# Kernel optimization log

Measured on AMD Instinct MI355X. Metric: run time of the kernel, lower is better.

The kernel has to match this reference:

```python
import jax, jax.numpy as jnp
import numpy as np

N_NODES = 100000


def gcn_conv(x, edge_index, W, b, n_nodes):
    """PyG GCNConv: add self-loops, symmetric deg^-1/2 normalization,
    linear transform, scatter-add aggregate, bias."""
    src, dst = edge_index[0], edge_index[1]
    # add self-loops
    loop = jnp.arange(n_nodes, dtype=edge_index.dtype)
    src = jnp.concatenate([src, loop])
    dst = jnp.concatenate([dst, loop])
    # transform first (in_dim >= out_dim ordering used by PyG)
    h = x @ W  # [N, out]
    # symmetric normalization from in-degree (incl. self-loops)
    ones = jnp.ones(src.shape[0], dtype=x.dtype)
    deg = jax.ops.segment_sum(ones, dst, num_segments=n_nodes)
    dinv = jnp.where(deg > 0, jax.lax.rsqrt(deg), 0.0).astype(x.dtype)
    norm = dinv[src] * dinv[dst]  # [E+N]
    msg = h[src] * norm[:, None]  # gather + scale
    out = jax.ops.segment_sum(msg, dst, num_segments=n_nodes)
    return out + b


def setup_inputs() -> dict:
    key = jax.random.key(0)
    k1, k2, k3, k4 = jax.random.split(key, 4)
    n, e = N_NODES, 1600000
    d_in, d_hid, n_cls = 256, 256, 64
    x = jax.random.normal(k1, (n, d_in), dtype=jnp.float32)
    edge_index = jax.random.randint(k2, (2, e), 0, n, dtype=jnp.int64)
    W1 = jax.random.normal(k3, (d_in, d_hid), dtype=jnp.float32) / np.sqrt(d_in)
    b1 = jnp.zeros((d_hid,), dtype=jnp.float32)
    W2 = jax.random.normal(k4, (d_hid, n_cls), dtype=jnp.float32) / np.sqrt(d_hid)
    b2 = jnp.zeros((n_cls,), dtype=jnp.float32)
    return {"x": x, "edge_index": edge_index, "W1": W1, "b1": b1, "W2": W2, "b2": b2}


def reference(x, edge_index, W1, b1, W2, b2):
    n = x.shape[0]
    h = jax.nn.relu(gcn_conv(x, edge_index, W1, b1, n))
    # dropout is identity in eval mode (training=False)
    logits = gcn_conv(h, edge_index, W2, b2, n)
    return jax.nn.log_softmax(logits, axis=1)
```

## Files before the change

kernel.cpp:

```cpp
#include <hip/hip_runtime.h>
#include <math.h>


typedef __attribute__((ext_vector_type(8))) short bf16x8;
typedef __attribute__((ext_vector_type(4))) float f32x4;

__device__ inline unsigned short f2bf(float f) {
    union { float f; unsigned int u; } v; v.f = f;
    unsigned int r = v.u + 0x7fffu + ((v.u >> 16) & 1u);
    return (unsigned short)(r >> 16);
}
__device__ inline float bf2f_lo(unsigned int u) {
    union { unsigned int u; float f; } v; v.u = u << 16; return v.f;
}
__device__ inline float bf2f_hi(unsigned int u) {
    union { unsigned int u; float f; } v; v.u = u & 0xffff0000u; return v.f;
}

__device__ inline void acc8(float* acc, uint4 q, float w) {
    acc[0] += bf2f_lo(q.x) * w; acc[1] += bf2f_hi(q.x) * w;
    acc[2] += bf2f_lo(q.y) * w; acc[3] += bf2f_hi(q.y) * w;
    acc[4] += bf2f_lo(q.z) * w; acc[5] += bf2f_hi(q.z) * w;
    acc[6] += bf2f_lo(q.w) * w; acc[7] += bf2f_hi(q.w) * w;
}

__global__ __launch_bounds__(256) void deg_count_kernel(
    const int* __restrict__ dst, int E, int* __restrict__ cnt) {
    int e = blockIdx.x * blockDim.x + threadIdx.x;
    if (e < E) atomicAdd(&cnt[dst[e]], 1);
}

__global__ __launch_bounds__(256) void scan_part1_kernel(
    const int* __restrict__ cnt, int* __restrict__ bsum, int N) {
    __shared__ int s[256];
    const int tid = threadIdx.x;
    int base = blockIdx.x * 1024 + tid * 4;
    int v = 0;
#pragma unroll
    for (int j = 0; j < 4; ++j)
        if (base + j < N) v += cnt[base + j];
    s[tid] = v;
    __syncthreads();
    for (int off = 128; off > 0; off >>= 1) {
        if (tid < off) s[tid] += s[tid + off];
        __syncthreads();
    }
    if (tid == 0) bsum[blockIdx.x] = s[0];
}

__global__ __launch_bounds__(1024) void scan_part2_kernel(
    const int* __restrict__ bsum, int* __restrict__ boffs, int NB,
    int* __restrict__ row_ptr, int N) {
    __shared__ int s[1024];
    const int tid = threadIdx.x;
    int v = (tid < NB) ? bsum[tid] : 0;
    s[tid] = v;
    __syncthreads();
    for (int off = 1; off < 1024; off <<= 1) {
        int t = (tid >= off) ? s[tid - off] : 0;
        __syncthreads();
        if (tid >= off) s[tid] += t;
        __syncthreads();
    }
    if (tid < NB) boffs[tid] = s[tid] - v;
    if (tid == 1023) row_ptr[N] = s[1023];
}

__global__ __launch_bounds__(256) void scan_part3_kernel(
    const int* __restrict__ cnt, const int* __restrict__ boffs,
    int* __restrict__ row_ptr, int* __restrict__ cursor, int N) {
    __shared__ int s[256];
    const int tid = threadIdx.x;
    int base = blockIdx.x * 1024 + tid * 4;
    int c[4];
    int v = 0;
#pragma unroll
    for (int j = 0; j < 4; ++j) {
        c[j] = (base + j < N) ? cnt[base + j] : 0;
        v += c[j];
    }
    s[tid] = v;
    __syncthreads();
    for (int off = 1; off < 256; off <<= 1) {
        int t = (tid >= off) ? s[tid - off] : 0;
        __syncthreads();
        if (tid >= off) s[tid] += t;
        __syncthreads();
    }
    int run = boffs[blockIdx.x] + s[tid] - v;
#pragma unroll
    for (int j = 0; j < 4; ++j) {
        if (base + j < N) {
            row_ptr[base + j] = run;
            cursor[base + j] = run;
            run += c[j];
        }
    }
}

__global__ __launch_bounds__(256) void scatter_kernel(
    const int* __restrict__ src, const int* __restrict__ dst,
    const int* __restrict__ cnt, int* __restrict__ cursor,
    int2* __restrict__ csr_ew, int E) {
    int e = blockIdx.x * blockDim.x + threadIdx.x;
    if (e >= E) return;
    int s = src[e], d = dst[e];
    float w = rsqrtf((float)cnt[s] + 1.0f) * rsqrtf((float)cnt[d] + 1.0f);
    int pos = atomicAdd(&cursor[d], 1);
    int2 rec;
    rec.x = s;
    rec.y = __float_as_int(w);
    csr_ew[pos] = rec;
}

__global__ __launch_bounds__(256) void castw_kernel(
    const float* __restrict__ W, unsigned short* __restrict__ Wt,
    int K, int Ncol) {
    int i = blockIdx.x * 256 + threadIdx.x;
    if (i < K * Ncol) {
        int n = i / K;
        int k = i - n * K;
        Wt[i] = f2bf(W[(size_t)k * Ncol + n]);
    }
}

__global__ __launch_bounds__(256) void gemm1_kernel(
    const float* __restrict__ A, const unsigned short* __restrict__ Bt,
    unsigned short* __restrict__ C, int M) {
    __shared__ unsigned short As[64][32];
    __shared__ unsigned short Bs[256][32];

    const int tid = threadIdx.x;
    const int wave = tid >> 6, lane = tid & 63;
    const int quad = lane >> 4, l15 = lane & 15;
    const int m0 = blockIdx.x * 64;

    f32x4 acc[4][4] = {};

    const int arow = tid >> 2;
    const int akk = (tid & 3) << 3;
    const int gr = m0 + arow;

    for (int k0 = 0; k0 < 256; k0 += 32) {
        float4 a0 = make_float4(0.f, 0.f, 0.f, 0.f), a1 = a0;
        if (gr < M) {
            a0 = *(const float4*)&A[(size_t)gr * 256 + k0 + akk];
            a1 = *(const float4*)&A[(size_t)gr * 256 + k0 + akk + 4];
        }
        bf16x8 av;
        av[0] = (short)f2bf(a0.x); av[1] = (short)f2bf(a0.y);
        av[2] = (short)f2bf(a0.z); av[3] = (short)f2bf(a0.w);
        av[4] = (short)f2bf(a1.x); av[5] = (short)f2bf(a1.y);
        av[6] = (short)f2bf(a1.z); av[7] = (short)f2bf(a1.w);
        *(bf16x8*)&As[arow][akk] = av;

        const unsigned short* bsrc = &Bt[(size_t)tid * 256 + k0];
        *(bf16x8*)&Bs[tid][0]  = *(const bf16x8*)&bsrc[0];
        *(bf16x8*)&Bs[tid][8]  = *(const bf16x8*)&bsrc[8];
        *(bf16x8*)&Bs[tid][16] = *(const bf16x8*)&bsrc[16];
        *(bf16x8*)&Bs[tid][24] = *(const bf16x8*)&bsrc[24];
        __syncthreads();

        bf16x8 af[4], bfv[4];
#pragma unroll
        for (int mt = 0; mt < 4; ++mt)
            af[mt] = *(const bf16x8*)&As[mt * 16 + l15][quad * 8];
#pragma unroll
        for (int nt = 0; nt < 4; ++nt)
            bfv[nt] = *(const bf16x8*)&Bs[wave * 64 + nt * 16 + l15][quad * 8];
#pragma unroll
        for (int mt = 0; mt < 4; ++mt)
#pragma unroll
            for (int nt = 0; nt < 4; ++nt)
                acc[mt][nt] = __builtin_amdgcn_mfma_f32_16x16x32_bf16(
                    af[mt], bfv[nt], acc[mt][nt], 0, 0, 0);
        __syncthreads();
    }

#pragma unroll
    for (int mt = 0; mt < 4; ++mt) {
#pragma unroll
        for (int nt = 0; nt < 4; ++nt) {
            int gcol = wave * 64 + nt * 16 + l15;
#pragma unroll
            for (int r = 0; r < 4; ++r) {
                int grow = m0 + mt * 16 + quad * 4 + r;
                if (grow < M)
                    C[(size_t)grow * 256 + gcol] = f2bf(acc[mt][nt][r]);
            }
        }
    }
}

__global__ __launch_bounds__(256) void agg256b_kernel(
    const uint4* __restrict__ h,
    const int2* __restrict__ ew,
    const int* __restrict__ row_ptr, const int* __restrict__ cnt,
    const float* __restrict__ bias, uint4* __restrict__ outb, int N) {
    const int node = blockIdx.x * 4 + (threadIdx.x >> 6);
    if (node >= N) return;
    const int lane = threadIdx.x & 63;
    const int half = lane >> 5;
    const int c = lane & 31;

    float dv = rsqrtf((float)cnt[node] + 1.0f);
    float w0 = dv * dv;

    float acc[8] = {0.f, 0.f, 0.f, 0.f, 0.f, 0.f, 0.f, 0.f};
    {
        uint4 q = h[(size_t)node * 32 + c];
        acc8(acc, q, half == 0 ? w0 : 0.f);
    }

    const int beg = row_ptr[node], end = row_ptr[node + 1];
    int e = beg;
    for (; e + 8 <= end; e += 8) {
        int2 r0 = ew[e + 0 + half];
        int2 r1 = ew[e + 2 + half];
        int2 r2 = ew[e + 4 + half];
        int2 r3 = ew[e + 6 + half];
        uint4 q0 = h[(size_t)r0.x * 32 + c];
        uint4 q1 = h[(size_t)r1.x * 32 + c];
        uint4 q2 = h[(size_t)r2.x * 32 + c];
        uint4 q3 = h[(size_t)r3.x * 32 + c];
        acc8(acc, q0, __int_as_float(r0.y));
        acc8(acc, q1, __int_as_float(r1.y));
        acc8(acc, q2, __int_as_float(r2.y));
        acc8(acc, q3, __int_as_float(r3.y));
    }
    for (; e < end; e += 2) {
        int idx = e + half;
        int idxc = min(idx, end - 1);
        int2 r = ew[idxc];
        float w = (idx < end) ? __int_as_float(r.y) : 0.f;
        uint4 q = h[(size_t)r.x * 32 + c];
        acc8(acc, q, w);
    }

#pragma unroll
    for (int k = 0; k < 8; ++k) acc[k] += __shfl_xor(acc[k], 32, 64);

    if (half == 0) {
        float4 b0 = *(const float4*)&bias[c * 8];
        float4 b1 = *(const float4*)&bias[c * 8 + 4];
        unsigned int o0 = f2bf(fmaxf(acc[0] + b0.x, 0.f));
        unsigned int o1 = f2bf(fmaxf(acc[1] + b0.y, 0.f));
        unsigned int o2 = f2bf(fmaxf(acc[2] + b0.z, 0.f));
        unsigned int o3 = f2bf(fmaxf(acc[3] + b0.w, 0.f));
        unsigned int o4 = f2bf(fmaxf(acc[4] + b1.x, 0.f));
        unsigned int o5 = f2bf(fmaxf(acc[5] + b1.y, 0.f));
        unsigned int o6 = f2bf(fmaxf(acc[6] + b1.z, 0.f));
        unsigned int o7 = f2bf(fmaxf(acc[7] + b1.w, 0.f));
        uint4 ov;
        ov.x = o0 | (o1 << 16);
        ov.y = o2 | (o3 << 16);
        ov.z = o4 | (o5 << 16);
        ov.w = o6 | (o7 << 16);
        outb[(size_t)node * 32 + c] = ov;
    }
}

__global__ __launch_bounds__(256) void gemm2_kernel(
    const unsigned short* __restrict__ Ab, const unsigned short* __restrict__ Bt,
    unsigned short* __restrict__ C, int M) {
    __shared__ unsigned short As[64][32];
    __shared__ unsigned short Bs[64][32];

    const int tid = threadIdx.x;
    const int wave = tid >> 6, lane = tid & 63;
    const int quad = lane >> 4, l15 = lane & 15;
    const int m0 = blockIdx.x * 64;

    f32x4 acc[4] = {};

    const int arow = tid >> 2;
    const int akk = (tid & 3) << 3;
    const int gr = m0 + arow;
    const int bn = tid & 63, bkc = (tid >> 6) << 3;

    for (int k0 = 0; k0 < 256; k0 += 32) {
        bf16x8 av = {};
        if (gr < M) av = *(const bf16x8*)&Ab[(size_t)gr * 256 + k0 + akk];
        *(bf16x8*)&As[arow][akk] = av;
        *(bf16x8*)&Bs[bn][bkc] = *(const bf16x8*)&Bt[(size_t)bn * 256 + k0 + bkc];
        __syncthreads();

        bf16x8 af = *(const bf16x8*)&As[wave * 16 + l15][quad * 8];
#pragma unroll
        for (int nt = 0; nt < 4; ++nt) {
            bf16x8 bfv = *(const bf16x8*)&Bs[nt * 16 + l15][quad * 8];
            acc[nt] = __builtin_amdgcn_mfma_f32_16x16x32_bf16(af, bfv, acc[nt], 0, 0, 0);
        }
        __syncthreads();
    }

#pragma unroll
    for (int nt = 0; nt < 4; ++nt) {
#pragma unroll
        for (int r = 0; r < 4; ++r) {
            int grow = m0 + wave * 16 + quad * 4 + r;
            if (grow < M) C[(size_t)grow * 64 + nt * 16 + l15] = f2bf(acc[nt][r]);
        }
    }
}

__global__ __launch_bounds__(256) void agg64_kernel(
    const uint4* __restrict__ h,
    const int2* __restrict__ ew, const int* __restrict__ row_ptr,
    const int* __restrict__ cnt, const float* __restrict__ bias,
    float* __restrict__ out, int N) {
    const int node = blockIdx.x * 4 + (threadIdx.x >> 6);
    if (node >= N) return;
    const int lane = threadIdx.x & 63;
    const int g = lane >> 3;
    const int c = lane & 7;

    float dv = rsqrtf((float)cnt[node] + 1.0f);
    float w0 = dv * dv;

    float acc[8] = {0.f, 0.f, 0.f, 0.f, 0.f, 0.f, 0.f, 0.f};
    {
        uint4 q = h[(size_t)node * 8 + c];
        acc8(acc, q, g == 0 ? w0 : 0.f);
    }

    const int beg = row_ptr[node], end = row_ptr[node + 1];
    int e = beg;
    for (; e + 16 <= end; e += 16) {
        int2 r0 = ew[e + g];
        int2 r1 = ew[e + 8 + g];
        uint4 q0 = h[(size_t)r0.x * 8 + c];
        uint4 q1 = h[(size_t)r1.x * 8 + c];
        acc8(acc, q0, __int_as_float(r0.y));
        acc8(acc, q1, __int_as_float(r1.y));
    }
    for (; e < end; e += 8) {
        int idx = e + g;
        int idxc = min(idx, end - 1);
        int2 r = ew[idxc];
        float w = (idx < end) ? __int_as_float(r.y) : 0.f;
        uint4 q = h[(size_t)r.x * 8 + c];
        acc8(acc, q, w);
    }

#pragma unroll
    for (int k = 0; k < 8; ++k) {
        acc[k] += __shfl_xor(acc[k], 8, 64);
        acc[k] += __shfl_xor(acc[k], 16, 64);
        acc[k] += __shfl_xor(acc[k], 32, 64);
    }

    float4 b0 = *(const float4*)&bias[c * 8];
    float4 b1 = *(const float4*)&bias[c * 8 + 4];
    float v[8];
    v[0] = acc[0] + b0.x; v[1] = acc[1] + b0.y;
    v[2] = acc[2] + b0.z; v[3] = acc[3] + b0.w;
    v[4] = acc[4] + b1.x; v[5] = acc[5] + b1.y;
    v[6] = acc[6] + b1.z; v[7] = acc[7] + b1.w;

    float m = v[0];
#pragma unroll
    for (int k = 1; k < 8; ++k) m = fmaxf(m, v[k]);
    m = fmaxf(m, __shfl_xor(m, 1, 64));
    m = fmaxf(m, __shfl_xor(m, 2, 64));
    m = fmaxf(m, __shfl_xor(m, 4, 64));
    float s = 0.f;
#pragma unroll
    for (int k = 0; k < 8; ++k) s += expf(v[k] - m);
    s += __shfl_xor(s, 1, 64);
    s += __shfl_xor(s, 2, 64);
    s += __shfl_xor(s, 4, 64);
    float ls = m + logf(s);

    if (g == 0) {
        float4 o0, o1;
        o0.x = v[0] - ls; o0.y = v[1] - ls; o0.z = v[2] - ls; o0.w = v[3] - ls;
        o1.x = v[4] - ls; o1.y = v[5] - ls; o1.z = v[6] - ls; o1.w = v[7] - ls;
        *(float4*)&out[(size_t)node * 64 + c * 8] = o0;
        *(float4*)&out[(size_t)node * 64 + c * 8 + 4] = o1;
    }
}

extern "C" void kernel_launch(void* const* d_in, const int* in_sizes, int n_in,
                              void* d_out, int out_size, void* d_ws, size_t ws_size,
                              hipStream_t stream) {
    const float* x  = (const float*)d_in[0];
    const int*   ei = (const int*)d_in[1];
    const float* W1 = (const float*)d_in[2];
    const float* b1 = (const float*)d_in[3];
    const float* W2 = (const float*)d_in[4];
    const float* b2 = (const float*)d_in[5];
    float* out = (float*)d_out;

    const int N = in_sizes[0] / 256;
    const int E = in_sizes[1] / 2;
    const int NP = 102400;
    const int NB = (N + 1023) / 1024;

    char* ws = (char*)d_ws;
    int*   cnt     = (int*)ws;                 ws += (size_t)NP * 4;
    int*   cursor  = (int*)ws;                 ws += (size_t)NP * 4;
    int*   row_ptr = (int*)ws;                 ws += (size_t)(NP + 4) * 4;
    int*   bsum    = (int*)ws;                 ws += (size_t)1024 * 4;
    int*   boffs   = (int*)ws;                 ws += (size_t)1024 * 4;
    int2*  csr_ew  = (int2*)ws;                ws += (size_t)E * 8;
    unsigned short* W1t   = (unsigned short*)ws; ws += (size_t)256 * 256 * 2;
    unsigned short* W2t   = (unsigned short*)ws; ws += (size_t)256 * 64 * 2;
    unsigned short* h1b   = (unsigned short*)ws; ws += (size_t)N * 256 * 2;
    unsigned short* agg1b = (unsigned short*)ws; ws += (size_t)N * 256 * 2;
    unsigned short* h2b   = (unsigned short*)ws; ws += (size_t)N * 64 * 2;

    hipMemsetAsync(cnt, 0, (size_t)N * sizeof(int), stream);

    deg_count_kernel<<<(E + 255) / 256, 256, 0, stream>>>(ei + E, E, cnt);
    scan_part1_kernel<<<NB, 256, 0, stream>>>(cnt, bsum, N);
    scan_part2_kernel<<<1, 1024, 0, stream>>>(bsum, boffs, NB, row_ptr, N);
    scan_part3_kernel<<<NB, 256, 0, stream>>>(cnt, boffs, row_ptr, cursor, N);
    scatter_kernel<<<(E + 255) / 256, 256, 0, stream>>>(
        ei, ei + E, cnt, cursor, csr_ew, E);

    castw_kernel<<<(256 * 256 + 255) / 256, 256, 0, stream>>>(W1, W1t, 256, 256);
    castw_kernel<<<(256 * 64 + 255) / 256, 256, 0, stream>>>(W2, W2t, 256, 64);

    const int mblocks = (N + 63) / 64;

    gemm1_kernel<<<mblocks, 256, 0, stream>>>(x, W1t, h1b, N);

    agg256b_kernel<<<(N + 3) / 4, 256, 0, stream>>>(
        (const uint4*)h1b, csr_ew, row_ptr, cnt, b1, (uint4*)agg1b, N);

    gemm2_kernel<<<mblocks, 256, 0, stream>>>(agg1b, W2t, h2b, N);

    agg64_kernel<<<(N + 3) / 4, 256, 0, stream>>>(
        (const uint4*)h2b, csr_ew, row_ptr, cnt, b2, out, N);
}
```

Baseline: 581.7 us.

## Record edge ranks during degree count, merge weight casts, widen GEMM1 tile

The degree-count kernel now stores each edge's atomic rank, so the CSR scatter computes its position as row_ptr plus rank instead of issuing a second atomic on a cursor array. The cursor buffer is removed and an E-sized rank buffer is added. The two weight-cast launches are merged into one kernel. GEMM1 now processes 128 rows per block instead of 64, reusing each B tile across more rows at the cost of more accumulator registers.

```diff
diff --git a/kernel.cpp b/kernel.cpp
--- a/kernel.cpp
+++ b/kernel.cpp
@@ -24,10 +24,11 @@
     acc[6] += bf2f_lo(q.w) * w; acc[7] += bf2f_hi(q.w) * w;
 }
 
-__global__ __launch_bounds__(256) void deg_count_kernel(
-    const int* __restrict__ dst, int E, int* __restrict__ cnt) {
+__global__ __launch_bounds__(256) void deg_rank_kernel(
+    const int* __restrict__ dst, int E, int* __restrict__ cnt,
+    int* __restrict__ rank) {
     int e = blockIdx.x * blockDim.x + threadIdx.x;
-    if (e < E) atomicAdd(&cnt[dst[e]], 1);
+    if (e < E) rank[e] = atomicAdd(&cnt[dst[e]], 1);
 }
 
 __global__ __launch_bounds__(256) void scan_part1_kernel(
@@ -68,7 +69,7 @@
 
 __global__ __launch_bounds__(256) void scan_part3_kernel(
     const int* __restrict__ cnt, const int* __restrict__ boffs,
-    int* __restrict__ row_ptr, int* __restrict__ cursor, int N) {
+    int* __restrict__ row_ptr, int N) {
     __shared__ int s[256];
     const int tid = threadIdx.x;
     int base = blockIdx.x * 1024 + tid * 4;
@@ -92,7 +93,6 @@
     for (int j = 0; j < 4; ++j) {
         if (base + j < N) {
             row_ptr[base + j] = run;
-            cursor[base + j] = run;
             run += c[j];
         }
     }
@@ -100,13 +100,13 @@
 
 __global__ __launch_bounds__(256) void scatter_kernel(
     const int* __restrict__ src, const int* __restrict__ dst,
-    const int* __restrict__ cnt, int* __restrict__ cursor,
-    int2* __restrict__ csr_ew, int E) {
+    const int* __restrict__ rank, const int* __restrict__ cnt,
+    const int* __restrict__ row_ptr, int2* __restrict__ csr_ew, int E) {
     int e = blockIdx.x * blockDim.x + threadIdx.x;
     if (e >= E) return;
     int s = src[e], d = dst[e];
     float w = rsqrtf((float)cnt[s] + 1.0f) * rsqrtf((float)cnt[d] + 1.0f);
-    int pos = atomicAdd(&cursor[d], 1);
+    int pos = row_ptr[d] + rank[e];
     int2 rec;
     rec.x = s;
     rec.y = __float_as_int(w);
@@ -114,45 +114,56 @@
 }
 
 __global__ __launch_bounds__(256) void castw_kernel(
-    const float* __restrict__ W, unsigned short* __restrict__ Wt,
-    int K, int Ncol) {
+    const float* __restrict__ W1, const float* __restrict__ W2,
+    unsigned short* __restrict__ W1t, unsigned short* __restrict__ W2t) {
     int i = blockIdx.x * 256 + threadIdx.x;
-    if (i < K * Ncol) {
-        int n = i / K;
-        int k = i - n * K;
-        Wt[i] = f2bf(W[(size_t)k * Ncol + n]);
+    if (i < 65536) {
+        int n = i >> 8, k = i & 255;
+        W1t[i] = f2bf(W1[(size_t)k * 256 + n]);
+    } else if (i < 65536 + 16384) {
+        int j = i - 65536;
+        int n = j >> 8, k = j & 255;
+        W2t[j] = f2bf(W2[(size_t)k * 64 + n]);
     }
 }
 
 __global__ __launch_bounds__(256) void gemm1_kernel(
     const float* __restrict__ A, const unsigned short* __restrict__ Bt,
     unsigned short* __restrict__ C, int M) {
-    __shared__ unsigned short As[64][32];
+    __shared__ unsigned short As[128][32];
     __shared__ unsigned short Bs[256][32];
 
     const int tid = threadIdx.x;
     const int wave = tid >> 6, lane = tid & 63;
     const int quad = lane >> 4, l15 = lane & 15;
-    const int m0 = blockIdx.x * 64;
-
-    f32x4 acc[4][4] = {};
-
-    const int arow = tid >> 2;
-    const int akk = (tid & 3) << 3;
+    const int m0 = blockIdx.x * 128;
+
+    f32x4 acc[8][4] = {};
+
+    const int arow = tid >> 1;
+    const int akk  = (tid & 1) << 4;
     const int gr = m0 + arow;
 
     for (int k0 = 0; k0 < 256; k0 += 32) {
-        float4 a0 = make_float4(0.f, 0.f, 0.f, 0.f), a1 = a0;
+        float4 a0 = make_float4(0.f,0.f,0.f,0.f), a1 = a0, a2 = a0, a3 = a0;
         if (gr < M) {
-            a0 = *(const float4*)&A[(size_t)gr * 256 + k0 + akk];
-            a1 = *(const float4*)&A[(size_t)gr * 256 + k0 + akk + 4];
-        }
-        bf16x8 av;
-        av[0] = (short)f2bf(a0.x); av[1] = (short)f2bf(a0.y);
-        av[2] = (short)f2bf(a0.z); av[3] = (short)f2bf(a0.w);
-        av[4] = (short)f2bf(a1.x); av[5] = (short)f2bf(a1.y);
-        av[6] = (short)f2bf(a1.z); av[7] = (short)f2bf(a1.w);
-        *(bf16x8*)&As[arow][akk] = av;
+            const float* ap = &A[(size_t)gr * 256 + k0 + akk];
+            a0 = *(const float4*)&ap[0];
+            a1 = *(const float4*)&ap[4];
+            a2 = *(const float4*)&ap[8];
+            a3 = *(const float4*)&ap[12];
+        }
+        bf16x8 av0, av1;
+        av0[0] = (short)f2bf(a0.x); av0[1] = (short)f2bf(a0.y);
+        av0[2] = (short)f2bf(a0.z); av0[3] = (short)f2bf(a0.w);
+        av0[4] = (short)f2bf(a1.x); av0[5] = (short)f2bf(a1.y);
+        av0[6] = (short)f2bf(a1.z); av0[7] = (short)f2bf(a1.w);
+        av1[0] = (short)f2bf(a2.x); av1[1] = (short)f2bf(a2.y);
+        av1[2] = (short)f2bf(a2.z); av1[3] = (short)f2bf(a2.w);
+        av1[4] = (short)f2bf(a3.x); av1[5] = (short)f2bf(a3.y);
+        av1[6] = (short)f2bf(a3.z); av1[7] = (short)f2bf(a3.w);
+        *(bf16x8*)&As[arow][akk]     = av0;
+        *(bf16x8*)&As[arow][akk + 8] = av1;
 
         const unsigned short* bsrc = &Bt[(size_t)tid * 256 + k0];
         *(bf16x8*)&Bs[tid][0]  = *(const bf16x8*)&bsrc[0];
@@ -161,24 +172,23 @@
         *(bf16x8*)&Bs[tid][24] = *(const bf16x8*)&bsrc[24];
         __syncthreads();
 
-        bf16x8 af[4], bfv[4];
-#pragma unroll
-        for (int mt = 0; mt < 4; ++mt)
-            af[mt] = *(const bf16x8*)&As[mt * 16 + l15][quad * 8];
+        bf16x8 bfv[4];
 #pragma unroll
         for (int nt = 0; nt < 4; ++nt)
             bfv[nt] = *(const bf16x8*)&Bs[wave * 64 + nt * 16 + l15][quad * 8];
 #pragma unroll
-        for (int mt = 0; mt < 4; ++mt)
+        for (int mt = 0; mt < 8; ++mt) {
+            bf16x8 af = *(const bf16x8*)&As[mt * 16 + l15][quad * 8];
 #pragma unroll
             for (int nt = 0; nt < 4; ++nt)
                 acc[mt][nt] = __builtin_amdgcn_mfma_f32_16x16x32_bf16(
-                    af[mt], bfv[nt], acc[mt][nt], 0, 0, 0);
-        __syncthreads();
-    }
-
-#pragma unroll
-    for (int mt = 0; mt < 4; ++mt) {
+                    af, bfv[nt], acc[mt][nt], 0, 0, 0);
+        }
+        __syncthreads();
+    }
+
+#pragma unroll
+    for (int mt = 0; mt < 8; ++mt) {
 #pragma unroll
         for (int nt = 0; nt < 4; ++nt) {
             int gcol = wave * 64 + nt * 16 + l15;
@@ -399,7 +409,7 @@
 
     char* ws = (char*)d_ws;
     int*   cnt     = (int*)ws;                 ws += (size_t)NP * 4;
-    int*   cursor  = (int*)ws;                 ws += (size_t)NP * 4;
+    int*   rank    = (int*)ws;                 ws += (size_t)E * 4;
     int*   row_ptr = (int*)ws;                 ws += (size_t)(NP + 4) * 4;
     int*   bsum    = (int*)ws;                 ws += (size_t)1024 * 4;
     int*   boffs   = (int*)ws;                 ws += (size_t)1024 * 4;
@@ -412,24 +422,21 @@
 
     hipMemsetAsync(cnt, 0, (size_t)N * sizeof(int), stream);
 
-    deg_count_kernel<<<(E + 255) / 256, 256, 0, stream>>>(ei + E, E, cnt);
+    deg_rank_kernel<<<(E + 255) / 256, 256, 0, stream>>>(ei + E, E, cnt, rank);
     scan_part1_kernel<<<NB, 256, 0, stream>>>(cnt, bsum, N);
     scan_part2_kernel<<<1, 1024, 0, stream>>>(bsum, boffs, NB, row_ptr, N);
-    scan_part3_kernel<<<NB, 256, 0, stream>>>(cnt, boffs, row_ptr, cursor, N);
+    scan_part3_kernel<<<NB, 256, 0, stream>>>(cnt, boffs, row_ptr, N);
     scatter_kernel<<<(E + 255) / 256, 256, 0, stream>>>(
-        ei, ei + E, cnt, cursor, csr_ew, E);
-
-    castw_kernel<<<(256 * 256 + 255) / 256, 256, 0, stream>>>(W1, W1t, 256, 256);
-    castw_kernel<<<(256 * 64 + 255) / 256, 256, 0, stream>>>(W2, W2t, 256, 64);
-
-    const int mblocks = (N + 63) / 64;
-
-    gemm1_kernel<<<mblocks, 256, 0, stream>>>(x, W1t, h1b, N);
+        ei, ei + E, rank, cnt, row_ptr, csr_ew, E);
+
+    castw_kernel<<<(65536 + 16384 + 255) / 256, 256, 0, stream>>>(W1, W2, W1t, W2t);
+
+    gemm1_kernel<<<(N + 127) / 128, 256, 0, stream>>>(x, W1t, h1b, N);
 
     agg256b_kernel<<<(N + 3) / 4, 256, 0, stream>>>(
         (const uint4*)h1b, csr_ew, row_ptr, cnt, b1, (uint4*)agg1b, N);
 
-    gemm2_kernel<<<mblocks, 256, 0, stream>>>(agg1b, W2t, h2b, N);
+    gemm2_kernel<<<(N + 63) / 64, 256, 0, stream>>>(agg1b, W2t, h2b, N);
 
     agg64_kernel<<<(N + 3) / 4, 256, 0, stream>>>(
         (const uint4*)h2b, csr_ew, row_ptr, cnt, b2, out, N);
```

New measurement: 554.4 us. -4.7%, faster.
